# Performance work log

Hardware: AMD Instinct MI355X
Metric: run time of the kernel (lower is better)

Reference implementation:

```python
import jax, jax.numpy as jnp
import numpy as np

N_VERTEX = 50000
N_EDGE = 400000
HV, HE, P, Q, MV, ME = 128, 64, 3, 3, 128, 128


def setup_inputs() -> dict:
    key = jax.random.key(0)
    ks = jax.random.split(key, 12)
    hv_ftr = jax.random.normal(ks[0], (N_VERTEX, HV), jnp.float32)
    he_ftr = jax.random.normal(ks[1], (N_EDGE, HE), jnp.float32)
    p_ftr = jax.random.normal(ks[2], (N_VERTEX, P), jnp.float32)
    q_ftr = jax.random.normal(ks[3], (N_VERTEX, Q), jnp.float32)
    edge_u = jax.random.randint(ks[4], (N_EDGE,), 0, N_VERTEX, jnp.int32)
    edge_v = jax.random.randint(ks[5], (N_EDGE,), 0, N_VERTEX, jnp.int32)
    # Linear params stored as [in, out] (y = x @ W + b), matching torch Linear math.
    Wa = jax.random.normal(ks[6], (HV, MV), jnp.float32) * 0.05      # attend
    ba = jnp.zeros((MV,), jnp.float32)
    Wal = jax.random.normal(ks[7], (P + Q + HE, 1), jnp.float32) * 0.05  # align
    bal = jnp.zeros((1,), jnp.float32)
    Wl = jax.random.normal(ks[8], (2 * HV + P + Q, ME), jnp.float32) * 0.05  # link
    bl = jnp.zeros((ME,), jnp.float32)
    return dict(hv_ftr=hv_ftr, he_ftr=he_ftr, p_ftr=p_ftr, q_ftr=q_ftr,
                edge_u=edge_u, edge_v=edge_v,
                Wa=Wa, ba=ba, Wal=Wal, bal=bal, Wl=Wl, bl=bl)


def reference(hv_ftr, he_ftr, p_ftr, q_ftr, edge_u, edge_v, Wa, ba, Wal, bal, Wl, bl):
    # dropout is p=0.0 (identity). The dense vew/veb matmuls in the torch code
    # are exactly gathers / a per-vertex (segment) softmax / scatter-adds.
    E = he_ftr.shape[0]
    N = hv_ftr.shape[0]
    # bidirectionalize: vew_u = cat([vew1, vew2]), vew_v = cat([vew2, vew1])
    u = jnp.concatenate([edge_u, edge_v])  # [2E] source of each directed edge
    v = jnp.concatenate([edge_v, edge_u])  # [2E] destination

    hv_u = hv_ftr[u]                       # vew_u.T @ hv_ftr
    hv_v = hv_ftr[v]                       # vew_v.T @ hv_ftr
    p_uv = p_ftr[v] - p_ftr[u]
    q_uv = q_ftr[v] - q_ftr[u]
    he2 = jnp.concatenate([he_ftr, he_ftr], axis=0)

    attend = jax.nn.leaky_relu(hv_v @ Wa + ba)                       # [2E, MV]
    scores = (jnp.concatenate([p_uv, q_uv, he2], axis=1) @ Wal + bal).reshape(-1)  # [2E]

    # per-destination-vertex softmax over incident directed edges
    # (equals dense softmax of vew_v @ diag(scores) + veb_v with -inf mask bias)
    smax = jax.lax.stop_gradient(jax.ops.segment_max(scores, v, num_segments=N))
    ex = jnp.exp(scores - smax[v])
    denom = jax.ops.segment_sum(ex, v, num_segments=N)
    align = ex / denom[v]                                            # [2E]

    mv_ftr = jax.nn.elu(jax.ops.segment_sum(align[:, None] * attend, v, num_segments=N))  # [N, MV]

    me2 = jnp.concatenate([hv_u, p_uv, q_uv, hv_v], axis=1) @ Wl + bl  # [2E, ME]
    me_ftr = jax.nn.leaky_relu(me2[:E] + me2[E:])                      # [E, ME]
    return mv_ftr, me_ftr
```

## Files before the change

### kernel.cpp

```cpp
#include <hip/hip_runtime.h>
#include <math.h>

typedef unsigned short u16;
typedef __attribute__((ext_vector_type(8))) short short8;
typedef __attribute__((ext_vector_type(4))) float f32x4;

__device__ __forceinline__ u16 f2b(float f) {
    unsigned u = __float_as_uint(f);
    u += 0x7fffu + ((u >> 16) & 1u);
    return (u16)(u >> 16);
}

__device__ __forceinline__ short8 cvt8(const f32x4* __restrict__ p) {
    f32x4 a = p[0], b = p[1];
    short8 r;
    r[0] = (short)f2b(a[0]); r[1] = (short)f2b(a[1]);
    r[2] = (short)f2b(a[2]); r[3] = (short)f2b(a[3]);
    r[4] = (short)f2b(b[0]); r[5] = (short)f2b(b[1]);
    r[6] = (short)f2b(b[2]); r[7] = (short)f2b(b[3]);
    return r;
}

__global__ __launch_bounds__(256) void k_prep(
    const float* __restrict__ hv, const float* __restrict__ Wa, const float* __restrict__ Wl,
    u16* __restrict__ hvb, u16* __restrict__ WpT, u16* __restrict__ WaT,
    unsigned char* __restrict__ mark, int NV, int nbHV)
{
    if ((int)blockIdx.x < nbHV) {
        size_t base = (size_t)blockIdx.x * 2048 + (size_t)threadIdx.x * 8;
        if (base + 8 <= (size_t)NV * 128) {
            short8 r = cvt8((const f32x4*)(hv + base));
            *(short8*)(hvb + base) = r;
        }
        int r0 = (int)blockIdx.x * 16 + (int)threadIdx.x;
        if (threadIdx.x < 16 && r0 < NV) mark[r0] = 0;
    } else {
        int c = ((int)blockIdx.x - nbHV) * 2 + ((int)threadIdx.x >> 7);
        int k = threadIdx.x & 127;
        WaT[c * 128 + k] = f2b(Wa[k * 128 + c]);
        WpT[c * 128 + k] = f2b(Wl[k * 128 + c] + Wl[(134 + k) * 128 + c]);
    }
}

__global__ void k_mark(const int* __restrict__ eu, const int* __restrict__ ev,
                       unsigned char* __restrict__ mark, int NE)
{
    int i = blockIdx.x * 256 + threadIdx.x;
    if (i < NE) { mark[eu[i]] = 1; mark[ev[i]] = 1; }
}

__global__ __launch_bounds__(256) void k_main(
    const u16* __restrict__ hvb, const float* __restrict__ hv,
    const int* __restrict__ eu, const int* __restrict__ ev,
    const u16* __restrict__ WpT, const u16* __restrict__ WaT,
    const float* __restrict__ bl, const float* __restrict__ ba,
    const unsigned char* __restrict__ mark,
    float* __restrict__ mv_out, float* __restrict__ me_out,
    int NE, int NV, int nbE)
{
    const int lane = threadIdx.x & 63;
    const int wv   = threadIdx.x >> 6;
    const int m = lane & 15, q = lane >> 4;

    if ((int)blockIdx.x < nbE) {
        const int e0 = blockIdx.x * 64 + wv * 16;
        int e = e0 + m; if (e >= NE) e = NE - 1;
        const int iu = eu[e];
        const int iv = ev[e];

        short8 au[4], av[4];
        {
            const short8* up = (const short8*)(hvb + (size_t)iu * 128 + q * 8);
            const short8* vp = (const short8*)(hvb + (size_t)iv * 128 + q * 8);
            #pragma unroll
            for (int ks = 0; ks < 4; ++ks) { au[ks] = up[ks * 4]; av[ks] = vp[ks * 4]; }
        }

        f32x4 acc[8];
        #pragma unroll
        for (int t = 0; t < 8; ++t) acc[t] = (f32x4){0.f, 0.f, 0.f, 0.f};

        #pragma unroll
        for (int ks = 0; ks < 4; ++ks) {
            short8 b[8];
            #pragma unroll
            for (int t = 0; t < 8; ++t)
                b[t] = *(const short8*)(WpT + (size_t)(t * 16 + m) * 128 + ks * 32 + q * 8);
            #pragma unroll
            for (int t = 0; t < 8; ++t)
                acc[t] = __builtin_amdgcn_mfma_f32_16x16x32_bf16(au[ks], b[t], acc[t], 0, 0, 0);
            #pragma unroll
            for (int t = 0; t < 8; ++t)
                acc[t] = __builtin_amdgcn_mfma_f32_16x16x32_bf16(av[ks], b[t], acc[t], 0, 0, 0);
        }

        #pragma unroll
        for (int t = 0; t < 8; ++t) {
            const int col  = t * 16 + m;
            const float bias = 2.0f * bl[col];
            #pragma unroll
            for (int i = 0; i < 4; ++i) {
                const int row = e0 + q * 4 + i;
                if (row < NE) {
                    float x = acc[t][i] + bias;
                    x = (x > 0.f) ? x : 0.01f * x;
                    __builtin_nontemporal_store(x, &me_out[(size_t)row * 128 + col]);
                }
            }
        }
    } else {
        const int vb = (int)blockIdx.x - nbE;
        const int n0 = vb * 64 + wv * 16;
        int nl = n0 + m; if (nl >= NV) nl = NV - 1;

        short8 a[4];
        {
            const f32x4* ap = (const f32x4*)(hv + (size_t)nl * 128 + q * 8);
            #pragma unroll
            for (int ks = 0; ks < 4; ++ks) a[ks] = cvt8(ap + ks * 8);
        }

        f32x4 acc[8];
        #pragma unroll
        for (int t = 0; t < 8; ++t) acc[t] = (f32x4){0.f, 0.f, 0.f, 0.f};

        #pragma unroll
        for (int ks = 0; ks < 4; ++ks) {
            #pragma unroll
            for (int t = 0; t < 8; ++t) {
                short8 b = *(const short8*)(WaT + (size_t)(t * 16 + m) * 128 + ks * 32 + q * 8);
                acc[t] = __builtin_amdgcn_mfma_f32_16x16x32_bf16(a[ks], b, acc[t], 0, 0, 0);
            }
        }

        #pragma unroll
        for (int t = 0; t < 8; ++t) {
            const int col  = t * 16 + m;
            const float bias = ba[col];
            #pragma unroll
            for (int i = 0; i < 4; ++i) {
                const int row = n0 + q * 4 + i;
                if (row < NV) {
                    float z = acc[t][i] + bias;
                    float y = (z > 0.f) ? z : 0.01f * z;
                    float r = (y > 0.f) ? y : (__expf(y) - 1.f);
                    if (mark[row] == 0) r = 0.f;
                    __builtin_nontemporal_store(r, &mv_out[(size_t)row * 128 + col]);
                }
            }
        }
    }
}

extern "C" void kernel_launch(void* const* d_in, const int* in_sizes, int n_in,
                              void* d_out, int out_size, void* d_ws, size_t ws_size,
                              hipStream_t stream)
{
    const float* hv = (const float*)d_in[0];
    const int*   eu = (const int*)d_in[4];
    const int*   ev = (const int*)d_in[5];
    const float* Wa = (const float*)d_in[6];
    const float* ba = (const float*)d_in[7];
    const float* Wl = (const float*)d_in[10];
    const float* bl = (const float*)d_in[11];

    const int NV = in_sizes[0] / 128;
    const int NE = in_sizes[4];

    float* mv_out = (float*)d_out;
    float* me_out = mv_out + (size_t)NV * 128;

    const int nbHV = (NV * 128 + 2047) / 2048;
    const int nbE  = (NE + 63) / 64;
    const int nbV  = (NV + 63) / 64;

    const size_t hvb_bytes = (size_t)NV * 128 * 2;
    const size_t need_ws   = hvb_bytes + 128 * 128 * 2 * 2 + (size_t)NV;

    if (ws_size >= need_ws) {
        u16* hvb = (u16*)d_ws;
        u16* WpT = hvb + (size_t)NV * 128;
        u16* WaT = WpT + 128 * 128;
        unsigned char* mark = (unsigned char*)(WaT + 128 * 128);

        k_prep<<<nbHV + 64, 256, 0, stream>>>(hv, Wa, Wl, hvb, WpT, WaT, mark, NV, nbHV);
        k_mark<<<(NE + 255) / 256, 256, 0, stream>>>(eu, ev, mark, NE);
        k_main<<<nbE + nbV, 256, 0, stream>>>(hvb, hv, eu, ev, WpT, WaT, bl, ba, mark,
                                              mv_out, me_out, NE, NV, nbE);
    } else {
        u16* hvb = (u16*)mv_out;
        u16* WpT = (u16*)d_ws;
        u16* WaT = WpT + 128 * 128;
        unsigned char* mark = (unsigned char*)(WaT + 128 * 128);

        k_prep<<<nbHV + 64, 256, 0, stream>>>(hv, Wa, Wl, hvb, WpT, WaT, mark, NV, nbHV);
        k_mark<<<(NE + 255) / 256, 256, 0, stream>>>(eu, ev, mark, NE);
        k_main<<<nbE, 256, 0, stream>>>(hvb, hv, eu, ev, WpT, WaT, bl, ba, mark,
                                        mv_out, me_out, NE, NV, nbE);
        k_main<<<nbV, 256, 0, stream>>>(hvb, hv, eu, ev, WpT, WaT, bl, ba, mark,
                                        mv_out, me_out, NE, NV, 0);
    }
}
```

Measured before the change: 426.9 us.

## Precompute per-vertex link projection and gather-add per edge instead of per-edge GEMM

The link matmul is linear, so (hv_u+hv_v)@Wp equals hv_u@Wp + hv_v@Wp. The change computes hv@Wp once per vertex (fused with the attend GEMM) into a workspace table. A light edge kernel then gathers two 512-byte rows per edge, adds them and applies leaky ReLU. This replaces the per-edge MFMA work and the bf16 hv conversion pass with a per-vertex GEMM plus gathers. When workspace is short it falls back to a bf16 table, which adds rounding error.

```diff
diff --git a/kernel.cpp b/kernel.cpp
--- a/kernel.cpp
+++ b/kernel.cpp
@@ -3,12 +3,17 @@
 
 typedef unsigned short u16;
 typedef __attribute__((ext_vector_type(8))) short short8;
+typedef __attribute__((ext_vector_type(4))) short short4v;
 typedef __attribute__((ext_vector_type(4))) float f32x4;
 
 __device__ __forceinline__ u16 f2b(float f) {
     unsigned u = __float_as_uint(f);
     u += 0x7fffu + ((u >> 16) & 1u);
     return (u16)(u >> 16);
+}
+
+__device__ __forceinline__ float b2f(u16 u) {
+    return __uint_as_float(((unsigned)u) << 16);
 }
 
 __device__ __forceinline__ short8 cvt8(const f32x4* __restrict__ p) {
@@ -22,20 +27,15 @@
 }
 
 __global__ __launch_bounds__(256) void k_prep(
-    const float* __restrict__ hv, const float* __restrict__ Wa, const float* __restrict__ Wl,
-    u16* __restrict__ hvb, u16* __restrict__ WpT, u16* __restrict__ WaT,
-    unsigned char* __restrict__ mark, int NV, int nbHV)
-{
-    if ((int)blockIdx.x < nbHV) {
-        size_t base = (size_t)blockIdx.x * 2048 + (size_t)threadIdx.x * 8;
-        if (base + 8 <= (size_t)NV * 128) {
-            short8 r = cvt8((const f32x4*)(hv + base));
-            *(short8*)(hvb + base) = r;
-        }
-        int r0 = (int)blockIdx.x * 16 + (int)threadIdx.x;
-        if (threadIdx.x < 16 && r0 < NV) mark[r0] = 0;
+    const float* __restrict__ Wa, const float* __restrict__ Wl,
+    u16* __restrict__ WpT, u16* __restrict__ WaT,
+    unsigned* __restrict__ markw, int nWords, int nbM)
+{
+    if ((int)blockIdx.x < nbM) {
+        int i = (int)blockIdx.x * 256 + (int)threadIdx.x;
+        if (i < nWords) markw[i] = 0u;
     } else {
-        int c = ((int)blockIdx.x - nbHV) * 2 + ((int)threadIdx.x >> 7);
+        int c = ((int)blockIdx.x - nbM) * 2 + ((int)threadIdx.x >> 7);
         int k = threadIdx.x & 127;
         WaT[c * 128 + k] = f2b(Wa[k * 128 + c]);
         WpT[c * 128 + k] = f2b(Wl[k * 128 + c] + Wl[(134 + k) * 128 + c]);
@@ -49,105 +49,159 @@
     if (i < NE) { mark[eu[i]] = 1; mark[ev[i]] = 1; }
 }
 
-__global__ __launch_bounds__(256) void k_main(
-    const u16* __restrict__ hvb, const float* __restrict__ hv,
-    const int* __restrict__ eu, const int* __restrict__ ev,
+__global__ __launch_bounds__(256) void k_vgemm(
+    const float* __restrict__ hv,
     const u16* __restrict__ WpT, const u16* __restrict__ WaT,
     const float* __restrict__ bl, const float* __restrict__ ba,
     const unsigned char* __restrict__ mark,
-    float* __restrict__ mv_out, float* __restrict__ me_out,
-    int NE, int NV, int nbE)
+    float* __restrict__ mv_out, float* __restrict__ yl32, u16* __restrict__ ylb,
+    int NV, int mode)
 {
     const int lane = threadIdx.x & 63;
     const int wv   = threadIdx.x >> 6;
     const int m = lane & 15, q = lane >> 4;
-
-    if ((int)blockIdx.x < nbE) {
-        const int e0 = blockIdx.x * 64 + wv * 16;
-        int e = e0 + m; if (e >= NE) e = NE - 1;
-        const int iu = eu[e];
-        const int iv = ev[e];
-
-        short8 au[4], av[4];
-        {
-            const short8* up = (const short8*)(hvb + (size_t)iu * 128 + q * 8);
-            const short8* vp = (const short8*)(hvb + (size_t)iv * 128 + q * 8);
-            #pragma unroll
-            for (int ks = 0; ks < 4; ++ks) { au[ks] = up[ks * 4]; av[ks] = vp[ks * 4]; }
-        }
-
-        f32x4 acc[8];
+    const int n0 = (int)blockIdx.x * 64 + wv * 16;
+    int nl = n0 + m; if (nl >= NV) nl = NV - 1;
+
+    short8 a[4];
+    {
+        const f32x4* ap = (const f32x4*)(hv + (size_t)nl * 128 + q * 8);
         #pragma unroll
-        for (int t = 0; t < 8; ++t) acc[t] = (f32x4){0.f, 0.f, 0.f, 0.f};
-
-        #pragma unroll
-        for (int ks = 0; ks < 4; ++ks) {
-            short8 b[8];
-            #pragma unroll
-            for (int t = 0; t < 8; ++t)
-                b[t] = *(const short8*)(WpT + (size_t)(t * 16 + m) * 128 + ks * 32 + q * 8);
-            #pragma unroll
-            for (int t = 0; t < 8; ++t)
-                acc[t] = __builtin_amdgcn_mfma_f32_16x16x32_bf16(au[ks], b[t], acc[t], 0, 0, 0);
-            #pragma unroll
-            for (int t = 0; t < 8; ++t)
-                acc[t] = __builtin_amdgcn_mfma_f32_16x16x32_bf16(av[ks], b[t], acc[t], 0, 0, 0);
-        }
-
+        for (int ks = 0; ks < 4; ++ks) a[ks] = cvt8(ap + ks * 8);
+    }
+
+    f32x4 accA[8], accP[8];
+    #pragma unroll
+    for (int t = 0; t < 8; ++t) {
+        accA[t] = (f32x4){0.f, 0.f, 0.f, 0.f};
+        accP[t] = (f32x4){0.f, 0.f, 0.f, 0.f};
+    }
+
+    const bool doA = (mode & 1) != 0;
+    const bool doP = (mode & 6) != 0;
+
+    #pragma unroll
+    for (int ks = 0; ks < 4; ++ks) {
         #pragma unroll
         for (int t = 0; t < 8; ++t) {
-            const int col  = t * 16 + m;
-            const float bias = 2.0f * bl[col];
-            #pragma unroll
-            for (int i = 0; i < 4; ++i) {
-                const int row = e0 + q * 4 + i;
-                if (row < NE) {
-                    float x = acc[t][i] + bias;
-                    x = (x > 0.f) ? x : 0.01f * x;
-                    __builtin_nontemporal_store(x, &me_out[(size_t)row * 128 + col]);
-                }
-            }
-        }
-    } else {
-        const int vb = (int)blockIdx.x - nbE;
-        const int n0 = vb * 64 + wv * 16;
-        int nl = n0 + m; if (nl >= NV) nl = NV - 1;
-
-        short8 a[4];
-        {
-            const f32x4* ap = (const f32x4*)(hv + (size_t)nl * 128 + q * 8);
-            #pragma unroll
-            for (int ks = 0; ks < 4; ++ks) a[ks] = cvt8(ap + ks * 8);
-        }
-
-        f32x4 acc[8];
-        #pragma unroll
-        for (int t = 0; t < 8; ++t) acc[t] = (f32x4){0.f, 0.f, 0.f, 0.f};
-
-        #pragma unroll
-        for (int ks = 0; ks < 4; ++ks) {
-            #pragma unroll
-            for (int t = 0; t < 8; ++t) {
-                short8 b = *(const short8*)(WaT + (size_t)(t * 16 + m) * 128 + ks * 32 + q * 8);
-                acc[t] = __builtin_amdgcn_mfma_f32_16x16x32_bf16(a[ks], b, acc[t], 0, 0, 0);
-            }
-        }
-
-        #pragma unroll
-        for (int t = 0; t < 8; ++t) {
-            const int col  = t * 16 + m;
-            const float bias = ba[col];
+            const size_t rowoff = (size_t)(t * 16 + m) * 128 + ks * 32 + q * 8;
+            if (doA) {
+                short8 bfr = *(const short8*)(WaT + rowoff);
+                accA[t] = __builtin_amdgcn_mfma_f32_16x16x32_bf16(a[ks], bfr, accA[t], 0, 0, 0);
+            }
+            if (doP) {
+                short8 bfr = *(const short8*)(WpT + rowoff);
+                accP[t] = __builtin_amdgcn_mfma_f32_16x16x32_bf16(a[ks], bfr, accP[t], 0, 0, 0);
+            }
+        }
+    }
+
+    #pragma unroll
+    for (int t = 0; t < 8; ++t) {
+        const int col = t * 16 + m;
+        if (doA) {
+            const float bac = ba[col];
             #pragma unroll
             for (int i = 0; i < 4; ++i) {
                 const int row = n0 + q * 4 + i;
                 if (row < NV) {
-                    float z = acc[t][i] + bias;
+                    float z = accA[t][i] + bac;
                     float y = (z > 0.f) ? z : 0.01f * z;
                     float r = (y > 0.f) ? y : (__expf(y) - 1.f);
                     if (mark[row] == 0) r = 0.f;
                     __builtin_nontemporal_store(r, &mv_out[(size_t)row * 128 + col]);
                 }
             }
+        }
+        if (mode & 2) {
+            const float blc = bl[col];
+            #pragma unroll
+            for (int i = 0; i < 4; ++i) {
+                const int row = n0 + q * 4 + i;
+                if (row < NV) yl32[(size_t)row * 128 + col] = accP[t][i] + blc;
+            }
+        }
+        if (mode & 4) {
+            const float blc = bl[col];
+            #pragma unroll
+            for (int i = 0; i < 4; ++i) {
+                const int row = n0 + q * 4 + i;
+                if (row < NV) ylb[(size_t)row * 128 + col] = f2b(accP[t][i] + blc);
+            }
+        }
+    }
+}
+
+__global__ __launch_bounds__(256) void k_edge_f32(
+    const float* __restrict__ yl, const int* __restrict__ eu, const int* __restrict__ ev,
+    float* __restrict__ me, int NE)
+{
+    const int lane = threadIdx.x & 63;
+    const int wv   = threadIdx.x >> 6;
+    const int half = lane >> 5;
+    const int c4   = (lane & 31) << 2;
+    const int e0   = (int)blockIdx.x * 64 + wv * 16;
+
+    int iu[8], iv[8];
+    #pragma unroll
+    for (int j = 0; j < 8; ++j) {
+        int e = e0 + 2 * j + half; if (e >= NE) e = NE - 1;
+        iu[j] = eu[e]; iv[j] = ev[e];
+    }
+    f32x4 ru[8], rv[8];
+    #pragma unroll
+    for (int j = 0; j < 8; ++j) {
+        ru[j] = *(const f32x4*)(yl + (size_t)iu[j] * 128 + c4);
+        rv[j] = *(const f32x4*)(yl + (size_t)iv[j] * 128 + c4);
+    }
+    #pragma unroll
+    for (int j = 0; j < 8; ++j) {
+        int e = e0 + 2 * j + half;
+        if (e < NE) {
+            f32x4 o;
+            #pragma unroll
+            for (int i = 0; i < 4; ++i) {
+                float x = ru[j][i] + rv[j][i];
+                o[i] = (x > 0.f) ? x : 0.01f * x;
+            }
+            __builtin_nontemporal_store(o, (f32x4*)(me + (size_t)e * 128 + c4));
+        }
+    }
+}
+
+__global__ __launch_bounds__(256) void k_edge_b16(
+    const u16* __restrict__ ylb, const int* __restrict__ eu, const int* __restrict__ ev,
+    float* __restrict__ me, int NE)
+{
+    const int lane = threadIdx.x & 63;
+    const int wv   = threadIdx.x >> 6;
+    const int half = lane >> 5;
+    const int c4   = (lane & 31) << 2;
+    const int e0   = (int)blockIdx.x * 64 + wv * 16;
+
+    int iu[8], iv[8];
+    #pragma unroll
+    for (int j = 0; j < 8; ++j) {
+        int e = e0 + 2 * j + half; if (e >= NE) e = NE - 1;
+        iu[j] = eu[e]; iv[j] = ev[e];
+    }
+    short4v ru[8], rv[8];
+    #pragma unroll
+    for (int j = 0; j < 8; ++j) {
+        ru[j] = *(const short4v*)(ylb + (size_t)iu[j] * 128 + c4);
+        rv[j] = *(const short4v*)(ylb + (size_t)iv[j] * 128 + c4);
+    }
+    #pragma unroll
+    for (int j = 0; j < 8; ++j) {
+        int e = e0 + 2 * j + half;
+        if (e < NE) {
+            f32x4 o;
+            #pragma unroll
+            for (int i = 0; i < 4; ++i) {
+                float x = b2f((u16)ru[j][i]) + b2f((u16)rv[j][i]);
+                o[i] = (x > 0.f) ? x : 0.01f * x;
+            }
+            __builtin_nontemporal_store(o, (f32x4*)(me + (size_t)e * 128 + c4));
         }
     }
 }
@@ -170,34 +224,35 @@
     float* mv_out = (float*)d_out;
     float* me_out = mv_out + (size_t)NV * 128;
 
-    const int nbHV = (NV * 128 + 2047) / 2048;
-    const int nbE  = (NE + 63) / 64;
-    const int nbV  = (NV + 63) / 64;
-
-    const size_t hvb_bytes = (size_t)NV * 128 * 2;
-    const size_t need_ws   = hvb_bytes + 128 * 128 * 2 * 2 + (size_t)NV;
-
-    if (ws_size >= need_ws) {
-        u16* hvb = (u16*)d_ws;
-        u16* WpT = hvb + (size_t)NV * 128;
-        u16* WaT = WpT + 128 * 128;
-        unsigned char* mark = (unsigned char*)(WaT + 128 * 128);
-
-        k_prep<<<nbHV + 64, 256, 0, stream>>>(hv, Wa, Wl, hvb, WpT, WaT, mark, NV, nbHV);
-        k_mark<<<(NE + 255) / 256, 256, 0, stream>>>(eu, ev, mark, NE);
-        k_main<<<nbE + nbV, 256, 0, stream>>>(hvb, hv, eu, ev, WpT, WaT, bl, ba, mark,
-                                              mv_out, me_out, NE, NV, nbE);
+    u16* WpT = (u16*)d_ws;
+    u16* WaT = WpT + 128 * 128;
+    unsigned char* mark = (unsigned char*)(WaT + 128 * 128);
+    const size_t ylOff = 65536 + (((size_t)NV + 255) & ~(size_t)255);
+
+    const int nWords = (NV + 3) / 4;
+    const int nbM = (nWords + 255) / 256;
+    int nbV = (NV + 63) / 64; if (nbV < 1) nbV = 1;
+    int nbE = (NE + 63) / 64; if (nbE < 1) nbE = 1;
+
+    k_prep<<<nbM + 64, 256, 0, stream>>>(Wa, Wl, WpT, WaT, (unsigned*)mark, nWords, nbM);
+    k_mark<<<(NE + 255) / 256, 256, 0, stream>>>(eu, ev, mark, NE);
+
+    if (ws_size >= ylOff + (size_t)NV * 512) {
+        float* yl32 = (float*)((char*)d_ws + ylOff);
+        k_vgemm<<<nbV, 256, 0, stream>>>(hv, WpT, WaT, bl, ba, mark,
+                                         mv_out, yl32, nullptr, NV, 1 | 2);
+        k_edge_f32<<<nbE, 256, 0, stream>>>(yl32, eu, ev, me_out, NE);
+    } else if (ws_size >= ylOff + (size_t)NV * 256) {
+        u16* ylb = (u16*)((char*)d_ws + ylOff);
+        k_vgemm<<<nbV, 256, 0, stream>>>(hv, WpT, WaT, bl, ba, mark,
+                                         mv_out, nullptr, ylb, NV, 1 | 4);
+        k_edge_b16<<<nbE, 256, 0, stream>>>(ylb, eu, ev, me_out, NE);
     } else {
-        u16* hvb = (u16*)mv_out;
-        u16* WpT = (u16*)d_ws;
-        u16* WaT = WpT + 128 * 128;
-        unsigned char* mark = (unsigned char*)(WaT + 128 * 128);
-
-        k_prep<<<nbHV + 64, 256, 0, stream>>>(hv, Wa, Wl, hvb, WpT, WaT, mark, NV, nbHV);
-        k_mark<<<(NE + 255) / 256, 256, 0, stream>>>(eu, ev, mark, NE);
-        k_main<<<nbE, 256, 0, stream>>>(hvb, hv, eu, ev, WpT, WaT, bl, ba, mark,
-                                        mv_out, me_out, NE, NV, nbE);
-        k_main<<<nbV, 256, 0, stream>>>(hvb, hv, eu, ev, WpT, WaT, bl, ba, mark,
-                                        mv_out, me_out, NE, NV, 0);
-    }
-}
+        u16* ylb = (u16*)mv_out;
+        k_vgemm<<<nbV, 256, 0, stream>>>(hv, WpT, WaT, bl, ba, mark,
+                                         nullptr, nullptr, ylb, NV, 4);
+        k_edge_b16<<<nbE, 256, 0, stream>>>(ylb, eu, ev, me_out, NE);
+        k_vgemm<<<nbV, 256, 0, stream>>>(hv, WpT, WaT, bl, ba, mark,
+                                         mv_out, nullptr, nullptr, NV, 1);
+    }
+}
```

Result: slower. 588.8 us (+37.9%).
